# Optimization experiments

Measured on AMD Instinct MI355X. Metric: run time of the kernel, lower is better.

## Reference

```python
import jax, jax.numpy as jnp
import numpy as np

B, S, T = 4096, 2048, 2  # batch of conversations, turns per conversation, num_tags


def setup_inputs() -> dict:
    key = jax.random.key(0)
    k1, k2, k3, k4, k5, k6 = jax.random.split(key, 6)
    emissions = jax.random.normal(k1, (B, S, T), dtype=jnp.float32)
    # learned transition matrices for DistanceCRF branch order:
    # [even2odd, I0, D_consecutive, D_nonconsecutive]
    trans_params = jax.random.normal(k2, (4, T, T), dtype=jnp.float32) * 0.1
    tags = jax.random.randint(k3, (B, S), 0, T)
    who2who = jax.random.randint(k4, (B, S), 0, 2)
    intime = jax.random.randint(k5, (B, S), 0, 3)
    distance = jax.random.randint(k6, (B, S), 0, 4)
    return {"emissions": emissions, "trans_params": trans_params, "tags": tags,
            "who2who": who2who, "intime": intime, "distance": distance}


def _select_trans(trans_params, who2who, intime, distance):
    """Per-step transition matrix selection (DistanceCRF logic).
    Returns [B, S, T, T]."""
    Tn = trans_params.shape[-1]
    # index 0 = zero 'padding' matrix (who2who == -1 case)
    bank = jnp.concatenate([jnp.zeros((1, Tn, Tn), trans_params.dtype), trans_params], axis=0)
    sel = jnp.where(who2who == -1, 0,
          jnp.where(who2who == 1, 1,          # even2odd
          jnp.where(intime == 0, 2,           # I0
          jnp.where(distance == 0, 3, 4))))   # D_consecutive / D_nonconsecutive
    return bank[sel]


def reference(emissions, trans_params, tags, who2who, intime, distance):
    Bn, Sn, Tn = emissions.shape
    trans = _select_trans(trans_params, who2who, intime, distance)  # [B,S,T,T]

    # ---- gold path score ----
    em_gold = jnp.take_along_axis(emissions, tags[..., None], axis=-1)[..., 0].sum(-1)  # [B]
    oh_prev = jax.nn.one_hot(tags[:, :-1], Tn, dtype=emissions.dtype)  # [B,S-1,T]
    oh_cur = jax.nn.one_hot(tags[:, 1:], Tn, dtype=emissions.dtype)
    tr_gold = jnp.einsum('bsij,bsi,bsj->b', trans[:, 1:], oh_prev, oh_cur)  # [B]
    gold_score = em_gold + tr_gold

    # ---- log partition via forward recursion (note: transition added at t=0 too,
    # matching the original implementation) ----
    def step(alpha, xs):
        em_t, tr_t = xs  # [B,T], [B,T,T]
        new_alpha = jax.nn.logsumexp(alpha[:, :, None] + em_t[:, None, :] + tr_t, axis=1)
        return new_alpha, None

    alpha0 = jnp.zeros((Bn, Tn), emissions.dtype)
    xs = (jnp.swapaxes(emissions, 0, 1), jnp.swapaxes(trans, 0, 1))  # [S,B,T], [S,B,T,T]
    alpha, _ = jax.lax.scan(step, alpha0, xs)
    total_score = jax.nn.logsumexp(alpha, axis=-1)  # [B]

    return jnp.stack([gold_score, total_score])  # [2, B]
```

## Files before the change

### kernel.cpp

```cpp
#include <hip/hip_runtime.h>
#include <math.h>

#define Bn 4096
#define Sn 2048
#define BLOCK 256
#define CHUNK (Sn / BLOCK)

__device__ __forceinline__ float lse2(float a, float b) {
    float m = fmaxf(a, b);
    float d = fminf(a, b) - m;
    return m + __logf(1.0f + __expf(d));
}

struct Mat {
    float m00, m01, m10, m11;
};

__device__ __forceinline__ Mat compose(const Mat& P, const Mat& Q) {
    Mat r;
    r.m00 = lse2(P.m00 + Q.m00, P.m01 + Q.m10);
    r.m01 = lse2(P.m00 + Q.m01, P.m01 + Q.m11);
    r.m10 = lse2(P.m10 + Q.m00, P.m11 + Q.m10);
    r.m11 = lse2(P.m10 + Q.m01, P.m11 + Q.m11);
    return r;
}

__global__ __launch_bounds__(BLOCK) void crf_fwd(
    const float* __restrict__ emissions,
    const float* __restrict__ trans_params,
    const int*   __restrict__ tags,
    const int*   __restrict__ who2who,
    const int*   __restrict__ intime,
    const int*   __restrict__ distance,
    float*       __restrict__ out)
{
    const int b  = blockIdx.x;
    const int t  = threadIdx.x;
    const long base = (long)b * Sn;
    const int s0 = t * CHUNK;

    __shared__ __align__(16) float sbank[20];
    __shared__ float wm[4][5];

    if (t < 20) sbank[t] = (t < 4) ? 0.0f : trans_params[t - 4];
    __syncthreads();

    const int4* tp = (const int4*)(tags     + base) + t * 2;
    const int4* wp = (const int4*)(who2who  + base) + t * 2;
    const int4* ip = (const int4*)(intime   + base) + t * 2;
    const int4* dp = (const int4*)(distance + base) + t * 2;
    int4 ta = tp[0], tb = tp[1];
    int4 wa = wp[0], wb = wp[1];
    int4 ia = ip[0], ib = ip[1];
    int4 da = dp[0], db = dp[1];

    const float4* ep = (const float4*)(emissions + base * 2) + t * 4;
    float4 e0 = ep[0], e1 = ep[1], e2 = ep[2], e3 = ep[3];

    int tagv[CHUNK] = {ta.x, ta.y, ta.z, ta.w, tb.x, tb.y, tb.z, tb.w};
    int wv[CHUNK]   = {wa.x, wa.y, wa.z, wa.w, wb.x, wb.y, wb.z, wb.w};
    int iv[CHUNK]   = {ia.x, ia.y, ia.z, ia.w, ib.x, ib.y, ib.z, ib.w};
    int dv[CHUNK]   = {da.x, da.y, da.z, da.w, db.x, db.y, db.z, db.w};
    float emv[CHUNK][2] = {
        {e0.x, e0.y}, {e0.z, e0.w}, {e1.x, e1.y}, {e1.z, e1.w},
        {e2.x, e2.y}, {e2.z, e2.w}, {e3.x, e3.y}, {e3.z, e3.w}};

    int prev_tag = 0;
    if (t > 0) prev_tag = tags[base + s0 - 1];

    Mat M;
    float gold = 0.0f;

    #pragma unroll
    for (int k = 0; k < CHUNK; ++k) {
        int w = wv[k], it = iv[k], d = dv[k];
        int sel = (w == -1) ? 0 : (w == 1) ? 1 : (it == 0) ? 2 : (d == 0) ? 3 : 4;

        float4 trv = *(const float4*)(sbank + sel * 4);
        float t00 = trv.x, t01 = trv.y, t10 = trv.z, t11 = trv.w;
        float ek0 = emv[k][0], ek1 = emv[k][1];

        if (k == 0) {
            M.m00 = ek0 + t00; M.m01 = ek1 + t01;
            M.m10 = ek0 + t10; M.m11 = ek1 + t11;
        } else {
            float n00 = ek0 + lse2(M.m00 + t00, M.m01 + t10);
            float n01 = ek1 + lse2(M.m00 + t01, M.m01 + t11);
            float n10 = ek0 + lse2(M.m10 + t00, M.m11 + t10);
            float n11 = ek1 + lse2(M.m10 + t01, M.m11 + t11);
            M.m00 = n00; M.m01 = n01; M.m10 = n10; M.m11 = n11;
        }

        int tg = tagv[k];
        gold += tg ? ek1 : ek0;
        if (k > 0 || t > 0) {
            int pt = (k == 0) ? prev_tag : tagv[k - 1];
            float trg = pt ? (tg ? trv.w : trv.z) : (tg ? trv.y : trv.x);
            gold += trg;
        }
    }

    #pragma unroll
    for (int m = 1; m < 64; m <<= 1) {
        Mat O;
        O.m00 = __shfl_xor(M.m00, m);
        O.m01 = __shfl_xor(M.m01, m);
        O.m10 = __shfl_xor(M.m10, m);
        O.m11 = __shfl_xor(M.m11, m);
        float og = __shfl_xor(gold, m);
        bool upper = (t & m) != 0;
        Mat Lo = upper ? O : M;
        Mat Hi = upper ? M : O;
        M = compose(Lo, Hi);
        gold += og;
    }

    int wave = t >> 6;
    if ((t & 63) == 0) {
        wm[wave][0] = M.m00; wm[wave][1] = M.m01;
        wm[wave][2] = M.m10; wm[wave][3] = M.m11;
        wm[wave][4] = gold;
    }
    __syncthreads();

    if (t == 0) {
        Mat R = {wm[0][0], wm[0][1], wm[0][2], wm[0][3]};
        float g = wm[0][4];
        #pragma unroll
        for (int q = 1; q < 4; ++q) {
            Mat Q = {wm[q][0], wm[q][1], wm[q][2], wm[q][3]};
            R = compose(R, Q);
            g += wm[q][4];
        }
        float mx = fmaxf(fmaxf(R.m00, R.m01), fmaxf(R.m10, R.m11));
        float tot = mx + __logf(__expf(R.m00 - mx) + __expf(R.m01 - mx) +
                                __expf(R.m10 - mx) + __expf(R.m11 - mx));
        out[b]      = g;
        out[Bn + b] = tot;
    }
}

extern "C" void kernel_launch(void* const* d_in, const int* in_sizes, int n_in,
                              void* d_out, int out_size, void* d_ws, size_t ws_size,
                              hipStream_t stream) {
    const float* emissions    = (const float*)d_in[0];
    const float* trans_params = (const float*)d_in[1];
    const int*   tags         = (const int*)d_in[2];
    const int*   who2who      = (const int*)d_in[3];
    const int*   intime       = (const int*)d_in[4];
    const int*   distance     = (const int*)d_in[5];
    float* out = (float*)d_out;

    crf_fwd<<<dim3(Bn), dim3(BLOCK), 0, stream>>>(
        emissions, trans_params, tags, who2who, intime, distance, out);
}
```

Baseline: 205.2 us.

## Switch CRF recursion from log-space to linear-space with per-thread rescaling

Replaces the log-sum-exp max-plus matrix products with ordinary 2x2 products on exponentiated transitions and emissions. Each thread normalizes its 8-step chunk product by its max and carries a log scale, which is summed across the shuffle reduction. This removes most exp/log transcendental calls from the sequential chain and the reduction, leaving two exps per step. It risks underflow or overflow within an 8-step chunk and across the 64-lane product, since the reduction never renormalizes after the initial scaling.

```diff
diff --git a/kernel.cpp b/kernel.cpp
--- a/kernel.cpp
+++ b/kernel.cpp
@@ -5,25 +5,6 @@
 #define Sn 2048
 #define BLOCK 256
 #define CHUNK (Sn / BLOCK)
-
-__device__ __forceinline__ float lse2(float a, float b) {
-    float m = fmaxf(a, b);
-    float d = fminf(a, b) - m;
-    return m + __logf(1.0f + __expf(d));
-}
-
-struct Mat {
-    float m00, m01, m10, m11;
-};
-
-__device__ __forceinline__ Mat compose(const Mat& P, const Mat& Q) {
-    Mat r;
-    r.m00 = lse2(P.m00 + Q.m00, P.m01 + Q.m10);
-    r.m01 = lse2(P.m00 + Q.m01, P.m01 + Q.m11);
-    r.m10 = lse2(P.m10 + Q.m00, P.m11 + Q.m10);
-    r.m11 = lse2(P.m10 + Q.m01, P.m11 + Q.m11);
-    return r;
-}
 
 __global__ __launch_bounds__(BLOCK) void crf_fwd(
     const float* __restrict__ emissions,
@@ -39,10 +20,15 @@
     const long base = (long)b * Sn;
     const int s0 = t * CHUNK;
 
-    __shared__ __align__(16) float sbank[20];
-    __shared__ float wm[4][5];
+    __shared__ __align__(16) float lbank[20];
+    __shared__ __align__(16) float ebank[20];
+    __shared__ float wm[4][6];
 
-    if (t < 20) sbank[t] = (t < 4) ? 0.0f : trans_params[t - 4];
+    if (t < 20) {
+        float v = (t < 4) ? 0.0f : trans_params[t - 4];
+        lbank[t] = v;
+        ebank[t] = __expf(v);
+    }
     __syncthreads();
 
     const int4* tp = (const int4*)(tags     + base) + t * 2;
@@ -68,7 +54,7 @@
     int prev_tag = 0;
     if (t > 0) prev_tag = tags[base + s0 - 1];
 
-    Mat M;
+    float m00, m01, m10, m11;
     float gold = 0.0f;
 
     #pragma unroll
@@ -76,65 +62,78 @@
         int w = wv[k], it = iv[k], d = dv[k];
         int sel = (w == -1) ? 0 : (w == 1) ? 1 : (it == 0) ? 2 : (d == 0) ? 3 : 4;
 
-        float4 trv = *(const float4*)(sbank + sel * 4);
-        float t00 = trv.x, t01 = trv.y, t10 = trv.z, t11 = trv.w;
+        float4 P = *(const float4*)(ebank + sel * 4);
         float ek0 = emv[k][0], ek1 = emv[k][1];
+        float x0 = __expf(ek0), x1 = __expf(ek1);
 
         if (k == 0) {
-            M.m00 = ek0 + t00; M.m01 = ek1 + t01;
-            M.m10 = ek0 + t10; M.m11 = ek1 + t11;
+            m00 = P.x * x0; m01 = P.y * x1;
+            m10 = P.z * x0; m11 = P.w * x1;
         } else {
-            float n00 = ek0 + lse2(M.m00 + t00, M.m01 + t10);
-            float n01 = ek1 + lse2(M.m00 + t01, M.m01 + t11);
-            float n10 = ek0 + lse2(M.m10 + t00, M.m11 + t10);
-            float n11 = ek1 + lse2(M.m10 + t01, M.m11 + t11);
-            M.m00 = n00; M.m01 = n01; M.m10 = n10; M.m11 = n11;
+            float n00 = fmaf(m00, P.x, m01 * P.z) * x0;
+            float n01 = fmaf(m00, P.y, m01 * P.w) * x1;
+            float n10 = fmaf(m10, P.x, m11 * P.z) * x0;
+            float n11 = fmaf(m10, P.y, m11 * P.w) * x1;
+            m00 = n00; m01 = n01; m10 = n10; m11 = n11;
         }
 
         int tg = tagv[k];
         gold += tg ? ek1 : ek0;
         if (k > 0 || t > 0) {
             int pt = (k == 0) ? prev_tag : tagv[k - 1];
-            float trg = pt ? (tg ? trv.w : trv.z) : (tg ? trv.y : trv.x);
-            gold += trg;
+            gold += lbank[(sel << 2) + (pt << 1) + tg];
         }
     }
 
+    float mx  = fmaxf(fmaxf(m00, m01), fmaxf(m10, m11));
+    float inv = 1.0f / mx;
+    float L   = __logf(mx);
+    m00 *= inv; m01 *= inv; m10 *= inv; m11 *= inv;
+
     #pragma unroll
     for (int m = 1; m < 64; m <<= 1) {
-        Mat O;
-        O.m00 = __shfl_xor(M.m00, m);
-        O.m01 = __shfl_xor(M.m01, m);
-        O.m10 = __shfl_xor(M.m10, m);
-        O.m11 = __shfl_xor(M.m11, m);
-        float og = __shfl_xor(gold, m);
-        bool upper = (t & m) != 0;
-        Mat Lo = upper ? O : M;
-        Mat Hi = upper ? M : O;
-        M = compose(Lo, Hi);
+        float o00 = __shfl_xor(m00, m);
+        float o01 = __shfl_xor(m01, m);
+        float o10 = __shfl_xor(m10, m);
+        float o11 = __shfl_xor(m11, m);
+        float oL  = __shfl_xor(L, m);
+        float og  = __shfl_xor(gold, m);
+        bool up = (t & m) != 0;
+        float a00 = up ? o00 : m00, a01 = up ? o01 : m01;
+        float a10 = up ? o10 : m10, a11 = up ? o11 : m11;
+        float b00 = up ? m00 : o00, b01 = up ? m01 : o01;
+        float b10 = up ? m10 : o10, b11 = up ? m11 : o11;
+        m00 = fmaf(a00, b00, a01 * b10);
+        m01 = fmaf(a00, b01, a01 * b11);
+        m10 = fmaf(a10, b00, a11 * b10);
+        m11 = fmaf(a10, b01, a11 * b11);
+        L += oL;
         gold += og;
     }
 
     int wave = t >> 6;
     if ((t & 63) == 0) {
-        wm[wave][0] = M.m00; wm[wave][1] = M.m01;
-        wm[wave][2] = M.m10; wm[wave][3] = M.m11;
-        wm[wave][4] = gold;
+        wm[wave][0] = m00; wm[wave][1] = m01;
+        wm[wave][2] = m10; wm[wave][3] = m11;
+        wm[wave][4] = L;   wm[wave][5] = gold;
     }
     __syncthreads();
 
     if (t == 0) {
-        Mat R = {wm[0][0], wm[0][1], wm[0][2], wm[0][3]};
-        float g = wm[0][4];
+        float r00 = wm[0][0], r01 = wm[0][1], r10 = wm[0][2], r11 = wm[0][3];
+        float Ls = wm[0][4], g = wm[0][5];
         #pragma unroll
         for (int q = 1; q < 4; ++q) {
-            Mat Q = {wm[q][0], wm[q][1], wm[q][2], wm[q][3]};
-            R = compose(R, Q);
-            g += wm[q][4];
+            float q00 = wm[q][0], q01 = wm[q][1], q10 = wm[q][2], q11 = wm[q][3];
+            float n00 = fmaf(r00, q00, r01 * q10);
+            float n01 = fmaf(r00, q01, r01 * q11);
+            float n10 = fmaf(r10, q00, r11 * q10);
+            float n11 = fmaf(r10, q01, r11 * q11);
+            r00 = n00; r01 = n01; r10 = n10; r11 = n11;
+            Ls += wm[q][4];
+            g  += wm[q][5];
         }
-        float mx = fmaxf(fmaxf(R.m00, R.m01), fmaxf(R.m10, R.m11));
-        float tot = mx + __logf(__expf(R.m00 - mx) + __expf(R.m01 - mx) +
-                                __expf(R.m10 - mx) + __expf(R.m11 - mx));
+        float tot = Ls + __logf(r00 + r01 + r10 + r11);
         out[b]      = g;
         out[Bn + b] = tot;
     }
```

After: 202.4 us. No clear change (-1.4%).
